# Optimization experiments

Measured on AMD Instinct MI355X. Metric: run time of the kernel, lower is better.

Reference implementation:

```python
import jax, jax.numpy as jnp
import numpy as np

N = 50000      # nodes
E = 800000     # edges
IN = 128       # in_channels
HID = 128      # hidden_channels
R = 8          # num_relations
B = 4          # num_bases
EPS = 1e-5     # BatchNorm eps


def setup_inputs() -> dict:
    key = jax.random.key(0)
    ks = jax.random.split(key, 16)
    s = 0.05
    f = jnp.float32
    return {
        "x": jax.random.normal(ks[0], (N, IN), f),
        "edge_index": jax.random.randint(ks[1], (2, E), 0, N),
        "edge_type": jax.random.randint(ks[2], (E,), 0, R),
        # conv1 (RGCNConv with basis decomposition): W_r = sum_b comp[r,b] * bases[b]
        "comp1": jax.random.normal(ks[3], (R, B), f) * s,
        "bases1": jax.random.normal(ks[4], (B, IN, HID), f) * s,
        "root1": jax.random.normal(ks[5], (IN, HID), f) * s,
        "bias1": jnp.zeros((HID,), f),
        # skip1: Linear(in, hidden)
        "skip1_w": jax.random.normal(ks[6], (IN, HID), f) * s,
        "skip1_b": jnp.zeros((HID,), f),
        # BatchNorm(hidden)
        "bn_gamma": jnp.ones((HID,), f),
        "bn_beta": jnp.zeros((HID,), f),
        # conv2
        "comp2": jax.random.normal(ks[7], (R, B), f) * s,
        "bases2": jax.random.normal(ks[8], (B, HID, HID), f) * s,
        "root2": jax.random.normal(ks[9], (HID, HID), f) * s,
        "bias2": jnp.zeros((HID,), f),
        # skip2: Linear(hidden, hidden)
        "skip2_w": jax.random.normal(ks[10], (HID, HID), f) * s,
        "skip2_b": jnp.zeros((HID,), f),
    }


def rgcn_conv(x, src, dst, etype, comp, bases, root, bias):
    """PyG RGCNConv: per-relation mean aggregation + root weight + bias."""
    # Basis decomposition: W [R, d_in, d_out]
    W = jnp.einsum('rb,bdf->rdf', comp, bases)
    # Transform all nodes under every relation (node-level GEMM, avoids [E,B,F])
    h = jnp.einsum('nd,rdf->rnf', x, W)          # [R, N, F]
    msg = h[etype, src]                           # [E, F] gather per edge
    # mean per (dst, relation): normalize by relation-specific in-degree
    seg = dst * R + etype                         # combined segment id
    cnt = jax.ops.segment_sum(jnp.ones((msg.shape[0],), x.dtype), seg,
                              num_segments=N * R)
    msg = msg * (1.0 / jnp.maximum(cnt, 1.0))[seg][:, None]
    agg = jax.ops.segment_sum(msg, dst, num_segments=N)  # sum over relations
    return agg + x @ root + bias


def reference(x, edge_index, edge_type,
              comp1, bases1, root1, bias1, skip1_w, skip1_b,
              bn_gamma, bn_beta,
              comp2, bases2, root2, bias2, skip2_w, skip2_b):
    src, dst = edge_index[0], edge_index[1]
    # layer 1: conv + skip
    x1 = rgcn_conv(x, src, dst, edge_type, comp1, bases1, root1, bias1) \
         + x @ skip1_w + skip1_b
    h = x1  # captured pre-BatchNorm (i == num_layers - 1 branch)
    # BatchNorm (training-style batch stats) + ReLU; dropout = identity (eval)
    m = x1.mean(axis=0)
    v = x1.var(axis=0)
    xn = bn_gamma * (x1 - m) / jnp.sqrt(v + EPS) + bn_beta
    xr = jax.nn.relu(xn)
    # final layer: conv + skip
    x2 = rgcn_conv(xr, src, dst, edge_type, comp2, bases2, root2, bias2) \
         + xr @ skip2_w + skip2_b
    return (h, x2)
```

## Files before the change

### kernel.cpp

```cpp
#include <hip/hip_runtime.h>
#include <hip/hip_bf16.h>

#define Nn   50000
#define Ee   800000
#define RR   8
#define CAP  96
#define EPSV 1e-5f

typedef unsigned int   u32;
typedef unsigned short u16;
typedef __attribute__((ext_vector_type(8))) short bf16x8;
typedef __attribute__((ext_vector_type(4))) float f32x4;

__device__ __forceinline__ float bf2f(u16 u) {
    return __uint_as_float(((u32)u) << 16);
}
__device__ __forceinline__ u16 f2bf(float f) {
    u32 x = __float_as_uint(f);
    u32 r = (x + 0x7FFFu + ((x >> 16) & 1u)) >> 16;
    return (u16)r;
}
__device__ __forceinline__ u32 pack2(float a, float b) {
    return (u32)f2bf(a) | ((u32)f2bf(b) << 16);
}

__global__ void __launch_bounds__(256) count_fill(const int* __restrict__ ei,
                                                  const int* __restrict__ et,
                                                  int* __restrict__ deg,
                                                  int* __restrict__ buckets) {
    int e = blockIdx.x * 256 + threadIdx.x;
    if (e >= Ee) return;
    int src = ei[e];
    int dst = ei[Ee + e];
    int rt  = et[e];
    int idx = atomicAdd(&deg[dst], 1);
    if (idx < CAP)
        __builtin_nontemporal_store((src & 0xFFFF) | (rt << 16),
                                    &buckets[dst * CAP + idx]);
}

__global__ void __launch_bounds__(256) cvt_bf16(const float2* __restrict__ xf,
                                                u32* __restrict__ xb) {
    int t = blockIdx.x * 256 + threadIdx.x;
    float2 v = xf[t];
    xb[t] = pack2(v.x, v.y);
}

__global__ void __launch_bounds__(256) prep_w(const float* __restrict__ bases,
                                              const float* __restrict__ root,
                                              const float* __restrict__ skipw,
                                              u16* __restrict__ wt) {
    int t = blockIdx.x * 256 + threadIdx.x;
    if (t >= 128 * 640) return;
    int c = t / 640, k = t % 640;
    float v;
    if (k < 512) {
        int b = k >> 7, kk = k & 127;
        v = bases[(b * 128 + kk) * 128 + c];
    } else {
        int kk = k - 512;
        v = root[kk * 128 + c] + skipw[kk * 128 + c];
    }
    wt[c * 640 + k] = f2bf(v);
}

__global__ void __launch_bounds__(256) aggregate(const u32* __restrict__ xrow,
                                                 const float* __restrict__ comp,
                                                 const int* __restrict__ deg,
                                                 const int* __restrict__ buckets,
                                                 u32* __restrict__ xcat) {
    __shared__ int   bk_s[4][CAP];
    __shared__ float scale_s[4][32];
    int wv = threadIdx.x >> 6, lane = threadIdx.x & 63;
    int node = blockIdx.x * 4 + wv;

    int d = deg[node];
    d = d < CAP ? d : CAP;
    const int* bk = buckets + node * CAP;

    int w0 = 0, w1 = 0;
    if (lane < d)      { w0 = bk[lane];      bk_s[wv][lane] = w0; }
    if (64 + lane < d) { w1 = bk[64 + lane]; bk_s[wv][64 + lane] = w1; }

    int rt0 = (lane < d) ? (w0 >> 16) : 8;
    int c[RR];
#pragma unroll
    for (int r = 0; r < RR; r++) c[r] = __popcll(__ballot(rt0 == r));
    for (int i = 64; i < d; i++) c[bk_s[wv][i] >> 16]++;

    if (lane < 32) {
        int r  = lane >> 2;
        int cc = c[r];
        float inv = 1.0f / (float)(cc < 1 ? 1 : cc);
        scale_s[wv][lane] = comp[lane] * inv;
    }
    __syncthreads();

    float a0 = 0, a1 = 0, b0 = 0, b1 = 0, c0 = 0, c1 = 0, d0 = 0, d1 = 0;
    int i = 0;
    for (; i + 4 <= d; i += 4) {
        int e0 = bk_s[wv][i], e1 = bk_s[wv][i + 1];
        int e2 = bk_s[wv][i + 2], e3 = bk_s[wv][i + 3];
        u32 x0 = xrow[(e0 & 0xFFFF) * 64 + lane];
        u32 x1 = xrow[(e1 & 0xFFFF) * 64 + lane];
        u32 x2 = xrow[(e2 & 0xFFFF) * 64 + lane];
        u32 x3 = xrow[(e3 & 0xFFFF) * 64 + lane];
        f32x4 s0 = *(const f32x4*)&scale_s[wv][(e0 >> 16) * 4];
        f32x4 s1 = *(const f32x4*)&scale_s[wv][(e1 >> 16) * 4];
        f32x4 s2 = *(const f32x4*)&scale_s[wv][(e2 >> 16) * 4];
        f32x4 s3 = *(const f32x4*)&scale_s[wv][(e3 >> 16) * 4];
        float v0, v1;
        v0 = bf2f((u16)x0); v1 = bf2f((u16)(x0 >> 16));
        a0 += s0[0] * v0; a1 += s0[0] * v1; b0 += s0[1] * v0; b1 += s0[1] * v1;
        c0 += s0[2] * v0; c1 += s0[2] * v1; d0 += s0[3] * v0; d1 += s0[3] * v1;
        v0 = bf2f((u16)x1); v1 = bf2f((u16)(x1 >> 16));
        a0 += s1[0] * v0; a1 += s1[0] * v1; b0 += s1[1] * v0; b1 += s1[1] * v1;
        c0 += s1[2] * v0; c1 += s1[2] * v1; d0 += s1[3] * v0; d1 += s1[3] * v1;
        v0 = bf2f((u16)x2); v1 = bf2f((u16)(x2 >> 16));
        a0 += s2[0] * v0; a1 += s2[0] * v1; b0 += s2[1] * v0; b1 += s2[1] * v1;
        c0 += s2[2] * v0; c1 += s2[2] * v1; d0 += s2[3] * v0; d1 += s2[3] * v1;
        v0 = bf2f((u16)x3); v1 = bf2f((u16)(x3 >> 16));
        a0 += s3[0] * v0; a1 += s3[0] * v1; b0 += s3[1] * v0; b1 += s3[1] * v1;
        c0 += s3[2] * v0; c1 += s3[2] * v1; d0 += s3[3] * v0; d1 += s3[3] * v1;
    }
    for (; i < d; i++) {
        int ee = bk_s[wv][i];
        u32 xv = xrow[(ee & 0xFFFF) * 64 + lane];
        f32x4 ss = *(const f32x4*)&scale_s[wv][(ee >> 16) * 4];
        float v0 = bf2f((u16)xv), v1 = bf2f((u16)(xv >> 16));
        a0 += ss[0] * v0; a1 += ss[0] * v1; b0 += ss[1] * v0; b1 += ss[1] * v1;
        c0 += ss[2] * v0; c1 += ss[2] * v1; d0 += ss[3] * v0; d1 += ss[3] * v1;
    }

    u32* orow = xcat + node * 320;
    orow[0 * 64 + lane] = pack2(a0, a1);
    orow[1 * 64 + lane] = pack2(b0, b1);
    orow[2 * 64 + lane] = pack2(c0, c1);
    orow[3 * 64 + lane] = pack2(d0, d1);
    orow[256 + lane]    = xrow[node * 64 + lane];
}

#define LDK 40
__global__ void __launch_bounds__(256) gemm_x(const u16* __restrict__ xcat,
                                              const u16* __restrict__ wt,
                                              const float* __restrict__ biasA,
                                              const float* __restrict__ biasB,
                                              float* __restrict__ out,
                                              float* __restrict__ bnsum,
                                              int do_stats) {
    __shared__ char smem_raw[64 * 129 * 4];
    u16*   As = (u16*)smem_raw;
    u16*   Bs = (u16*)(smem_raw + 64 * LDK * 2);
    float* Ct = (float*)smem_raw;

    int t = threadIdx.x;
    int w = t >> 6, lane = t & 63;
    int m0 = blockIdx.x * 64;

    f32x4 acc[8];
#pragma unroll
    for (int i = 0; i < 8; i++) acc[i] = (f32x4){0, 0, 0, 0};

    int arow = t >> 2, akof = (t & 3) * 8;
    int ar_frag = (w * 16 + (lane & 15)) * LDK + (lane >> 4) * 8;

    for (int ks = 0; ks < 20; ks++) {
        int k0 = ks * 32;
        uint4 av = {0, 0, 0, 0};
        int grow = m0 + arow;
        if (grow < Nn) av = *(const uint4*)(xcat + grow * 640 + k0 + akof);
        *(uint4*)(As + arow * LDK + akof) = av;
#pragma unroll
        for (int j = 0; j < 2; j++) {
            int cid = t + j * 256;
            int col = cid >> 2, kof = (cid & 3) * 8;
            uint4 bv = *(const uint4*)(wt + col * 640 + k0 + kof);
            *(uint4*)(Bs + col * LDK + kof) = bv;
        }
        __syncthreads();
        bf16x8 af = *(const bf16x8*)(As + ar_frag);
#pragma unroll
        for (int tt = 0; tt < 8; tt++) {
            bf16x8 bfr = *(const bf16x8*)(Bs + (tt * 16 + (lane & 15)) * LDK + (lane >> 4) * 8);
            acc[tt] = __builtin_amdgcn_mfma_f32_16x16x32_bf16(af, bfr, acc[tt], 0, 0, 0);
        }
        __syncthreads();
    }

#pragma unroll
    for (int tt = 0; tt < 8; tt++)
#pragma unroll
        for (int i = 0; i < 4; i++) {
            int row = w * 16 + (lane >> 4) * 4 + i;
            int col = tt * 16 + (lane & 15);
            Ct[row * 129 + col] = acc[tt][i];
        }
    __syncthreads();

    int ct = t & 127;
    float bias = biasA[ct] + biasB[ct];
    float lsum = 0, lsq = 0;
#pragma unroll 4
    for (int j = 0; j < 32; j++) {
        int row  = 2 * j + (t >> 7);
        int grow = m0 + row;
        if (grow < Nn) {
            float v = Ct[row * 129 + ct] + bias;
            out[grow * 128 + ct] = v;
            lsum += v;
            lsq  += v * v;
        }
    }
    if (do_stats) {
        atomicAdd(&bnsum[ct], lsum);
        atomicAdd(&bnsum[128 + ct], lsq);
    }
}

__global__ void bn_final(const float* __restrict__ bnsum,
                         const float* __restrict__ gamma,
                         const float* __restrict__ beta,
                         float* __restrict__ ab) {
    int c = threadIdx.x;
    float m   = bnsum[c] * (1.0f / Nn);
    float ex2 = bnsum[128 + c] * (1.0f / Nn);
    float var = ex2 - m * m;
    float s   = gamma[c] / sqrtf(var + EPSV);
    ab[c]       = s;
    ab[128 + c] = beta[c] - m * s;
}

__global__ void __launch_bounds__(256) bn_relu(const float2* __restrict__ h,
                                               const float* __restrict__ ab,
                                               u32* __restrict__ xr) {
    int t = blockIdx.x * 256 + threadIdx.x;
    int c0 = (t & 63) * 2;
    float2 hv = h[t];
    float v0 = hv.x * ab[c0] + ab[128 + c0];
    float v1 = hv.y * ab[c0 + 1] + ab[128 + c0 + 1];
    v0 = v0 > 0.f ? v0 : 0.f;
    v1 = v1 > 0.f ? v1 : 0.f;
    xr[t] = pack2(v0, v1);
}

extern "C" void kernel_launch(void* const* d_in, const int* in_sizes, int n_in,
                              void* d_out, int out_size, void* d_ws, size_t ws_size,
                              hipStream_t stream) {
    const float* x      = (const float*)d_in[0];
    const int*   ei     = (const int*)d_in[1];
    const int*   et     = (const int*)d_in[2];
    const float* comp1  = (const float*)d_in[3];
    const float* bases1 = (const float*)d_in[4];
    const float* root1  = (const float*)d_in[5];
    const float* bias1  = (const float*)d_in[6];
    const float* skip1w = (const float*)d_in[7];
    const float* skip1b = (const float*)d_in[8];
    const float* gamma  = (const float*)d_in[9];
    const float* beta   = (const float*)d_in[10];
    const float* comp2  = (const float*)d_in[11];
    const float* bases2 = (const float*)d_in[12];
    const float* root2  = (const float*)d_in[13];
    const float* bias2  = (const float*)d_in[14];
    const float* skip2w = (const float*)d_in[15];
    const float* skip2b = (const float*)d_in[16];
    float* out = (float*)d_out;

    char* ws = (char*)d_ws;
    int*   deg     = (int*)(ws + 0);
    float* bn      = (float*)(ws + 200000);
    float* ab      = (float*)(ws + 201216);
    int*   buckets = (int*)(ws + 202240);
    u16*   wt1     = (u16*)(ws + 19402240);
    u16*   wt2     = (u16*)(ws + 19566080);
    u32*   xb      = (u32*)(ws + 19729920);
    u32*   xr      = xb;
    u16*   xcat    = (u16*)(ws + 32529920);

    hipMemsetAsync(d_ws, 0, 201024, stream);

    count_fill<<<(Ee + 255) / 256, 256, 0, stream>>>(ei, et, deg, buckets);
    prep_w<<<320, 256, 0, stream>>>(bases1, root1, skip1w, wt1);
    prep_w<<<320, 256, 0, stream>>>(bases2, root2, skip2w, wt2);
    cvt_bf16<<<Nn / 4, 256, 0, stream>>>((const float2*)x, xb);

    aggregate<<<Nn / 4, 256, 0, stream>>>(xb, comp1, deg, buckets, (u32*)xcat);
    gemm_x<<<(Nn + 63) / 64, 256, 0, stream>>>(xcat, wt1, bias1, skip1b, out, bn, 1);

    bn_final<<<1, 128, 0, stream>>>(bn, gamma, beta, ab);
    bn_relu<<<Nn / 4, 256, 0, stream>>>((const float2*)out, ab, xr);

    aggregate<<<Nn / 4, 256, 0, stream>>>(xr, comp2, deg, buckets, (u32*)xcat);
    gemm_x<<<(Nn + 63) / 64, 256, 0, stream>>>(xcat, wt2, bias2, skip2b, out + Nn * 128, bn, 0);
}
```

Before: 352.1 us.

## Load GEMM fragments directly from global memory with 2x4 warp tiling

Removes the shared-memory staging of A and B tiles and the two barriers per k-step in gemm_x. Each wave now loads its MFMA fragments straight from global memory and computes a 32x64 sub-tile (2x4 MFMA tiles) instead of a 16x128 strip, giving more register reuse of each fragment. Out-of-range rows are clamped rather than zeroed. In exchange, operands that were shared across waves through LDS are now fetched separately by each wave, relying on cache hits, and the global loads are strided by row.

```diff
diff --git a/kernel.cpp b/kernel.cpp
--- a/kernel.cpp
+++ b/kernel.cpp
@@ -140,7 +140,6 @@
     orow[256 + lane]    = xrow[node * 64 + lane];
 }
 
-#define LDK 40
 __global__ void __launch_bounds__(256) gemm_x(const u16* __restrict__ xcat,
                                               const u16* __restrict__ wt,
                                               const float* __restrict__ biasA,
@@ -148,53 +147,60 @@
                                               float* __restrict__ out,
                                               float* __restrict__ bnsum,
                                               int do_stats) {
-    __shared__ char smem_raw[64 * 129 * 4];
-    u16*   As = (u16*)smem_raw;
-    u16*   Bs = (u16*)(smem_raw + 64 * LDK * 2);
-    float* Ct = (float*)smem_raw;
+    __shared__ float Ct[64 * 129];
 
     int t = threadIdx.x;
     int w = t >> 6, lane = t & 63;
     int m0 = blockIdx.x * 64;
-
-    f32x4 acc[8];
-#pragma unroll
-    for (int i = 0; i < 8; i++) acc[i] = (f32x4){0, 0, 0, 0};
-
-    int arow = t >> 2, akof = (t & 3) * 8;
-    int ar_frag = (w * 16 + (lane & 15)) * LDK + (lane >> 4) * 8;
-
+    int wr = (w & 1) * 32;
+    int wc = (w >> 1) * 64;
+
+    int r0 = m0 + wr + (lane & 15);
+    int r1 = r0 + 16;
+    r0 = r0 < Nn ? r0 : Nn - 1;
+    r1 = r1 < Nn ? r1 : Nn - 1;
+    const u16* ap0 = xcat + r0 * 640 + (lane >> 4) * 8;
+    const u16* ap1 = xcat + r1 * 640 + (lane >> 4) * 8;
+    const u16* bp0 = wt + (wc + (lane & 15)) * 640 + (lane >> 4) * 8;
+    const u16* bp1 = bp0 + 16 * 640;
+    const u16* bp2 = bp0 + 32 * 640;
+    const u16* bp3 = bp0 + 48 * 640;
+
+    f32x4 acc[2][4];
+#pragma unroll
+    for (int f = 0; f < 2; f++)
+#pragma unroll
+        for (int g = 0; g < 4; g++) acc[f][g] = (f32x4){0, 0, 0, 0};
+
+#pragma unroll 2
     for (int ks = 0; ks < 20; ks++) {
-        int k0 = ks * 32;
-        uint4 av = {0, 0, 0, 0};
-        int grow = m0 + arow;
-        if (grow < Nn) av = *(const uint4*)(xcat + grow * 640 + k0 + akof);
-        *(uint4*)(As + arow * LDK + akof) = av;
-#pragma unroll
-        for (int j = 0; j < 2; j++) {
-            int cid = t + j * 256;
-            int col = cid >> 2, kof = (cid & 3) * 8;
-            uint4 bv = *(const uint4*)(wt + col * 640 + k0 + kof);
-            *(uint4*)(Bs + col * LDK + kof) = bv;
-        }
-        __syncthreads();
-        bf16x8 af = *(const bf16x8*)(As + ar_frag);
-#pragma unroll
-        for (int tt = 0; tt < 8; tt++) {
-            bf16x8 bfr = *(const bf16x8*)(Bs + (tt * 16 + (lane & 15)) * LDK + (lane >> 4) * 8);
-            acc[tt] = __builtin_amdgcn_mfma_f32_16x16x32_bf16(af, bfr, acc[tt], 0, 0, 0);
-        }
-        __syncthreads();
-    }
-
-#pragma unroll
-    for (int tt = 0; tt < 8; tt++)
-#pragma unroll
-        for (int i = 0; i < 4; i++) {
-            int row = w * 16 + (lane >> 4) * 4 + i;
-            int col = tt * 16 + (lane & 15);
-            Ct[row * 129 + col] = acc[tt][i];
-        }
+        int ko = ks * 32;
+        bf16x8 a0 = *(const bf16x8*)(ap0 + ko);
+        bf16x8 a1 = *(const bf16x8*)(ap1 + ko);
+        bf16x8 b0 = *(const bf16x8*)(bp0 + ko);
+        bf16x8 b1 = *(const bf16x8*)(bp1 + ko);
+        bf16x8 b2 = *(const bf16x8*)(bp2 + ko);
+        bf16x8 b3 = *(const bf16x8*)(bp3 + ko);
+        acc[0][0] = __builtin_amdgcn_mfma_f32_16x16x32_bf16(a0, b0, acc[0][0], 0, 0, 0);
+        acc[1][0] = __builtin_amdgcn_mfma_f32_16x16x32_bf16(a1, b0, acc[1][0], 0, 0, 0);
+        acc[0][1] = __builtin_amdgcn_mfma_f32_16x16x32_bf16(a0, b1, acc[0][1], 0, 0, 0);
+        acc[1][1] = __builtin_amdgcn_mfma_f32_16x16x32_bf16(a1, b1, acc[1][1], 0, 0, 0);
+        acc[0][2] = __builtin_amdgcn_mfma_f32_16x16x32_bf16(a0, b2, acc[0][2], 0, 0, 0);
+        acc[1][2] = __builtin_amdgcn_mfma_f32_16x16x32_bf16(a1, b2, acc[1][2], 0, 0, 0);
+        acc[0][3] = __builtin_amdgcn_mfma_f32_16x16x32_bf16(a0, b3, acc[0][3], 0, 0, 0);
+        acc[1][3] = __builtin_amdgcn_mfma_f32_16x16x32_bf16(a1, b3, acc[1][3], 0, 0, 0);
+    }
+
+#pragma unroll
+    for (int f = 0; f < 2; f++)
+#pragma unroll
+        for (int g = 0; g < 4; g++)
+#pragma unroll
+            for (int i = 0; i < 4; i++) {
+                int row = wr + f * 16 + (lane >> 4) * 4 + i;
+                int col = wc + g * 16 + (lane & 15);
+                Ct[row * 129 + col] = acc[f][g][i];
+            }
     __syncthreads();
 
     int ct = t & 127;
```

New measurement: 401.7 us. 1.14x slower.

## Fuse aggregation and GEMM into one per-layer kernel via shared memory

Applied to the files above, without the earlier changes.

Merges the gather/aggregate kernel and the MFMA GEMM into a single rgcn_layer kernel. Aggregated basis features for 32 nodes are kept in LDS instead of being written to a global xcat buffer and read back. The root/skip part reads x rows directly from global memory, and the weight fragments are loaded straight from global/L2 with no LDS staging. Edge indices are broadcast via shuffles rather than LDS. This removes the xcat round-trip and one launch per layer, at the cost of each 4-wave block serially gathering 8 nodes per wave and re-reading the full weight matrix per 32-row tile.

```diff
diff --git a/kernel.cpp b/kernel.cpp
--- a/kernel.cpp
+++ b/kernel.cpp
@@ -6,6 +6,8 @@
 #define RR   8
 #define CAP  96
 #define EPSV 1e-5f
+#define MT   32
+#define LDA  520
 
 typedef unsigned int   u32;
 typedef unsigned short u16;
@@ -64,136 +66,127 @@
     wt[c * 640 + k] = f2bf(v);
 }
 
-__global__ void __launch_bounds__(256) aggregate(const u32* __restrict__ xrow,
-                                                 const float* __restrict__ comp,
-                                                 const int* __restrict__ deg,
-                                                 const int* __restrict__ buckets,
-                                                 u32* __restrict__ xcat) {
-    __shared__ int   bk_s[4][CAP];
+__global__ void __launch_bounds__(256) rgcn_layer(const u32* __restrict__ xrow,
+                                                  const float* __restrict__ comp,
+                                                  const int* __restrict__ deg,
+                                                  const int* __restrict__ buckets,
+                                                  const u16* __restrict__ wt,
+                                                  const float* __restrict__ biasA,
+                                                  const float* __restrict__ biasB,
+                                                  float* __restrict__ out,
+                                                  float* __restrict__ bnsum,
+                                                  int do_stats) {
+    __shared__ u16   As[MT * LDA];
     __shared__ float scale_s[4][32];
-    int wv = threadIdx.x >> 6, lane = threadIdx.x & 63;
-    int node = blockIdx.x * 4 + wv;
-
-    int d = deg[node];
-    d = d < CAP ? d : CAP;
-    const int* bk = buckets + node * CAP;
-
-    int w0 = 0, w1 = 0;
-    if (lane < d)      { w0 = bk[lane];      bk_s[wv][lane] = w0; }
-    if (64 + lane < d) { w1 = bk[64 + lane]; bk_s[wv][64 + lane] = w1; }
-
-    int rt0 = (lane < d) ? (w0 >> 16) : 8;
-    int c[RR];
-#pragma unroll
-    for (int r = 0; r < RR; r++) c[r] = __popcll(__ballot(rt0 == r));
-    for (int i = 64; i < d; i++) c[bk_s[wv][i] >> 16]++;
-
-    if (lane < 32) {
-        int r  = lane >> 2;
-        int cc = c[r];
-        float inv = 1.0f / (float)(cc < 1 ? 1 : cc);
-        scale_s[wv][lane] = comp[lane] * inv;
+    float* Ct = (float*)As;
+
+    int t = threadIdx.x, w = t >> 6, lane = t & 63;
+    int m0 = blockIdx.x * MT;
+
+    for (int ni = 0; ni < 8; ni++) {
+        int row  = w * 8 + ni;
+        int node = m0 + row;
+        if (node >= Nn) break;
+        int d = deg[node];
+        d = d < CAP ? d : CAP;
+        const int* bk = buckets + node * CAP;
+        int w0 = 0, w1 = 0;
+        if (lane < d)      w0 = bk[lane];
+        if (64 + lane < d) w1 = bk[64 + lane];
+
+        int rt0 = (lane < d) ? (w0 >> 16) : 8;
+        int c[RR];
+#pragma unroll
+        for (int r = 0; r < RR; r++) c[r] = __popcll(__ballot(rt0 == r));
+        if (d > 64)
+            for (int i = 64; i < d; i++) c[(__shfl(w1, i - 64) >> 16) & 7]++;
+
+        if (lane < 32) {
+            int cc = c[lane >> 2];
+            scale_s[w][lane] = comp[lane] / (float)(cc < 1 ? 1 : cc);
+        }
+
+        float a0 = 0, a1 = 0, b0 = 0, b1 = 0, c0 = 0, c1 = 0, d0 = 0, d1 = 0;
+        int i = 0;
+        if (d <= 64) {
+            for (; i + 8 <= d; i += 8) {
+                u32 g[8]; f32x4 s[8];
+#pragma unroll
+                for (int j = 0; j < 8; j++) {
+                    int e = __shfl(w0, i + j);
+                    g[j]  = xrow[(e & 0xFFFF) * 64 + lane];
+                    s[j]  = *(const f32x4*)&scale_s[w][((e >> 16) & 7) * 4];
+                }
+#pragma unroll
+                for (int j = 0; j < 8; j++) {
+                    float v0 = bf2f((u16)g[j]), v1 = bf2f((u16)(g[j] >> 16));
+                    a0 += s[j][0] * v0; a1 += s[j][0] * v1;
+                    b0 += s[j][1] * v0; b1 += s[j][1] * v1;
+                    c0 += s[j][2] * v0; c1 += s[j][2] * v1;
+                    d0 += s[j][3] * v0; d1 += s[j][3] * v1;
+                }
+            }
+        }
+        for (; i < d; i++) {
+            int e  = (i < 64) ? __shfl(w0, i) : __shfl(w1, i - 64);
+            u32 g  = xrow[(e & 0xFFFF) * 64 + lane];
+            f32x4 s = *(const f32x4*)&scale_s[w][((e >> 16) & 7) * 4];
+            float v0 = bf2f((u16)g), v1 = bf2f((u16)(g >> 16));
+            a0 += s[0] * v0; a1 += s[0] * v1; b0 += s[1] * v0; b1 += s[1] * v1;
+            c0 += s[2] * v0; c1 += s[2] * v1; d0 += s[3] * v0; d1 += s[3] * v1;
+        }
+
+        u32* arow = (u32*)As + row * (LDA / 2);
+        arow[0 * 64 + lane] = pack2(a0, a1);
+        arow[1 * 64 + lane] = pack2(b0, b1);
+        arow[2 * 64 + lane] = pack2(c0, c1);
+        arow[3 * 64 + lane] = pack2(d0, d1);
     }
     __syncthreads();
 
-    float a0 = 0, a1 = 0, b0 = 0, b1 = 0, c0 = 0, c1 = 0, d0 = 0, d1 = 0;
-    int i = 0;
-    for (; i + 4 <= d; i += 4) {
-        int e0 = bk_s[wv][i], e1 = bk_s[wv][i + 1];
-        int e2 = bk_s[wv][i + 2], e3 = bk_s[wv][i + 3];
-        u32 x0 = xrow[(e0 & 0xFFFF) * 64 + lane];
-        u32 x1 = xrow[(e1 & 0xFFFF) * 64 + lane];
-        u32 x2 = xrow[(e2 & 0xFFFF) * 64 + lane];
-        u32 x3 = xrow[(e3 & 0xFFFF) * 64 + lane];
-        f32x4 s0 = *(const f32x4*)&scale_s[wv][(e0 >> 16) * 4];
-        f32x4 s1 = *(const f32x4*)&scale_s[wv][(e1 >> 16) * 4];
-        f32x4 s2 = *(const f32x4*)&scale_s[wv][(e2 >> 16) * 4];
-        f32x4 s3 = *(const f32x4*)&scale_s[wv][(e3 >> 16) * 4];
-        float v0, v1;
-        v0 = bf2f((u16)x0); v1 = bf2f((u16)(x0 >> 16));
-        a0 += s0[0] * v0; a1 += s0[0] * v1; b0 += s0[1] * v0; b1 += s0[1] * v1;
-        c0 += s0[2] * v0; c1 += s0[2] * v1; d0 += s0[3] * v0; d1 += s0[3] * v1;
-        v0 = bf2f((u16)x1); v1 = bf2f((u16)(x1 >> 16));
-        a0 += s1[0] * v0; a1 += s1[0] * v1; b0 += s1[1] * v0; b1 += s1[1] * v1;
-        c0 += s1[2] * v0; c1 += s1[2] * v1; d0 += s1[3] * v0; d1 += s1[3] * v1;
-        v0 = bf2f((u16)x2); v1 = bf2f((u16)(x2 >> 16));
-        a0 += s2[0] * v0; a1 += s2[0] * v1; b0 += s2[1] * v0; b1 += s2[1] * v1;
-        c0 += s2[2] * v0; c1 += s2[2] * v1; d0 += s2[3] * v0; d1 += s2[3] * v1;
-        v0 = bf2f((u16)x3); v1 = bf2f((u16)(x3 >> 16));
-        a0 += s3[0] * v0; a1 += s3[0] * v1; b0 += s3[1] * v0; b1 += s3[1] * v1;
-        c0 += s3[2] * v0; c1 += s3[2] * v1; d0 += s3[3] * v0; d1 += s3[3] * v1;
-    }
-    for (; i < d; i++) {
-        int ee = bk_s[wv][i];
-        u32 xv = xrow[(ee & 0xFFFF) * 64 + lane];
-        f32x4 ss = *(const f32x4*)&scale_s[wv][(ee >> 16) * 4];
-        float v0 = bf2f((u16)xv), v1 = bf2f((u16)(xv >> 16));
-        a0 += ss[0] * v0; a1 += ss[0] * v1; b0 += ss[1] * v0; b1 += ss[1] * v1;
-        c0 += ss[2] * v0; c1 += ss[2] * v1; d0 += ss[3] * v0; d1 += ss[3] * v1;
-    }
-
-    u32* orow = xcat + node * 320;
-    orow[0 * 64 + lane] = pack2(a0, a1);
-    orow[1 * 64 + lane] = pack2(b0, b1);
-    orow[2 * 64 + lane] = pack2(c0, c1);
-    orow[3 * 64 + lane] = pack2(d0, d1);
-    orow[256 + lane]    = xrow[node * 64 + lane];
-}
-
-#define LDK 40
-__global__ void __launch_bounds__(256) gemm_x(const u16* __restrict__ xcat,
-                                              const u16* __restrict__ wt,
-                                              const float* __restrict__ biasA,
-                                              const float* __restrict__ biasB,
-                                              float* __restrict__ out,
-                                              float* __restrict__ bnsum,
-                                              int do_stats) {
-    __shared__ char smem_raw[64 * 129 * 4];
-    u16*   As = (u16*)smem_raw;
-    u16*   Bs = (u16*)(smem_raw + 64 * LDK * 2);
-    float* Ct = (float*)smem_raw;
-
-    int t = threadIdx.x;
-    int w = t >> 6, lane = t & 63;
-    int m0 = blockIdx.x * 64;
-
-    f32x4 acc[8];
-#pragma unroll
-    for (int i = 0; i < 8; i++) acc[i] = (f32x4){0, 0, 0, 0};
-
-    int arow = t >> 2, akof = (t & 3) * 8;
-    int ar_frag = (w * 16 + (lane & 15)) * LDK + (lane >> 4) * 8;
-
-    for (int ks = 0; ks < 20; ks++) {
-        int k0 = ks * 32;
-        uint4 av = {0, 0, 0, 0};
-        int grow = m0 + arow;
-        if (grow < Nn) av = *(const uint4*)(xcat + grow * 640 + k0 + akof);
-        *(uint4*)(As + arow * LDK + akof) = av;
-#pragma unroll
-        for (int j = 0; j < 2; j++) {
-            int cid = t + j * 256;
-            int col = cid >> 2, kof = (cid & 3) * 8;
-            uint4 bv = *(const uint4*)(wt + col * 640 + k0 + kof);
-            *(uint4*)(Bs + col * LDK + kof) = bv;
-        }
-        __syncthreads();
-        bf16x8 af = *(const bf16x8*)(As + ar_frag);
-#pragma unroll
-        for (int tt = 0; tt < 8; tt++) {
-            bf16x8 bfr = *(const bf16x8*)(Bs + (tt * 16 + (lane & 15)) * LDK + (lane >> 4) * 8);
-            acc[tt] = __builtin_amdgcn_mfma_f32_16x16x32_bf16(af, bfr, acc[tt], 0, 0, 0);
-        }
-        __syncthreads();
-    }
-
-#pragma unroll
-    for (int tt = 0; tt < 8; tt++)
+    int wr = (w & 1) * 16, wc = (w >> 1) * 64;
+    int lm = lane & 15, lk = (lane >> 4) * 8;
+    const u16* bp0 = wt + (wc + lm) * 640 + lk;
+    const u16* bp1 = bp0 + 16 * 640;
+    const u16* bp2 = bp0 + 32 * 640;
+    const u16* bp3 = bp0 + 48 * 640;
+
+    f32x4 acc[4];
+#pragma unroll
+    for (int g = 0; g < 4; g++) acc[g] = (f32x4){0, 0, 0, 0};
+
+    {
+        int r = m0 + wr + lm;
+        r = r < Nn ? r : Nn - 1;
+        const u16* ap = (const u16*)(xrow + r * 64) + lk;
+#pragma unroll
+        for (int g2 = 0; g2 < 4; g2++) {
+            bf16x8 a = *(const bf16x8*)(ap + g2 * 32);
+            int ko = 512 + g2 * 32;
+            acc[0] = __builtin_amdgcn_mfma_f32_16x16x32_bf16(a, *(const bf16x8*)(bp0 + ko), acc[0], 0, 0, 0);
+            acc[1] = __builtin_amdgcn_mfma_f32_16x16x32_bf16(a, *(const bf16x8*)(bp1 + ko), acc[1], 0, 0, 0);
+            acc[2] = __builtin_amdgcn_mfma_f32_16x16x32_bf16(a, *(const bf16x8*)(bp2 + ko), acc[2], 0, 0, 0);
+            acc[3] = __builtin_amdgcn_mfma_f32_16x16x32_bf16(a, *(const bf16x8*)(bp3 + ko), acc[3], 0, 0, 0);
+        }
+    }
+#pragma unroll 4
+    for (int ks = 0; ks < 16; ks++) {
+        bf16x8 a = *(const bf16x8*)(As + (wr + lm) * LDA + ks * 32 + lk);
+        int ko = ks * 32;
+        acc[0] = __builtin_amdgcn_mfma_f32_16x16x32_bf16(a, *(const bf16x8*)(bp0 + ko), acc[0], 0, 0, 0);
+        acc[1] = __builtin_amdgcn_mfma_f32_16x16x32_bf16(a, *(const bf16x8*)(bp1 + ko), acc[1], 0, 0, 0);
+        acc[2] = __builtin_amdgcn_mfma_f32_16x16x32_bf16(a, *(const bf16x8*)(bp2 + ko), acc[2], 0, 0, 0);
+        acc[3] = __builtin_amdgcn_mfma_f32_16x16x32_bf16(a, *(const bf16x8*)(bp3 + ko), acc[3], 0, 0, 0);
+    }
+    __syncthreads();
+
+#pragma unroll
+    for (int g = 0; g < 4; g++)
 #pragma unroll
         for (int i = 0; i < 4; i++) {
-            int row = w * 16 + (lane >> 4) * 4 + i;
-            int col = tt * 16 + (lane & 15);
-            Ct[row * 129 + col] = acc[tt][i];
+            int row = wr + (lane >> 4) * 4 + i;
+            int col = wc + g * 16 + lm;
+            Ct[row * 129 + col] = acc[g][i];
         }
     __syncthreads();
 
@@ -201,7 +194,7 @@
     float bias = biasA[ct] + biasB[ct];
     float lsum = 0, lsq = 0;
 #pragma unroll 4
-    for (int j = 0; j < 32; j++) {
+    for (int j = 0; j < 16; j++) {
         int row  = 2 * j + (t >> 7);
         int grow = m0 + row;
         if (grow < Nn) {
@@ -274,7 +267,6 @@
     u16*   wt2     = (u16*)(ws + 19566080);
     u32*   xb      = (u32*)(ws + 19729920);
     u32*   xr      = xb;
-    u16*   xcat    = (u16*)(ws + 32529920);
 
     hipMemsetAsync(d_ws, 0, 201024, stream);
 
@@ -283,12 +275,14 @@
     prep_w<<<320, 256, 0, stream>>>(bases2, root2, skip2w, wt2);
     cvt_bf16<<<Nn / 4, 256, 0, stream>>>((const float2*)x, xb);
 
-    aggregate<<<Nn / 4, 256, 0, stream>>>(xb, comp1, deg, buckets, (u32*)xcat);
-    gemm_x<<<(Nn + 63) / 64, 256, 0, stream>>>(xcat, wt1, bias1, skip1b, out, bn, 1);
+    int nblk = (Nn + MT - 1) / MT;
+
+    rgcn_layer<<<nblk, 256, 0, stream>>>(xb, comp1, deg, buckets, wt1,
+                                         bias1, skip1b, out, bn, 1);
 
     bn_final<<<1, 128, 0, stream>>>(bn, gamma, beta, ab);
     bn_relu<<<Nn / 4, 256, 0, stream>>>((const float2*)out, ab, xr);
 
-    aggregate<<<Nn / 4, 256, 0, stream>>>(xr, comp2, deg, buckets, (u32*)xcat);
-    gemm_x<<<(Nn + 63) / 64, 256, 0, stream>>>(xcat, wt2, bias2, skip2b, out + Nn * 128, bn, 0);
-}
+    rgcn_layer<<<nblk, 256, 0, stream>>>(xr, comp2, deg, buckets, wt2,
+                                         bias2, skip2b, out + Nn * 128, bn, 0);
+}
```

New measurement: 453.3 us. 28.8% more time.
